# Optimization experiments

Hardware: AMD Instinct MI355X
Metric: run time of the kernel (lower is better)

## Reference

```python
import jax, jax.numpy as jnp
import numpy as np

FIR_KERNEL = (1, 3, 3, 1)
FACTOR = 2


def _setup_kernel(k):
    k = np.asarray(k, dtype=np.float32)
    if k.ndim == 1:
        k = np.outer(k, k)
    k /= np.sum(k)
    return k


def _fir_filter_2d(x, kf, pad0, pad1):
    # upfirdn2d with up=down=1: pad then depthwise-correlate with flipped FIR kernel.
    # x: [N, H, W, C], kf: [kh, kw]
    C = x.shape[3]
    x = jnp.pad(x, ((0, 0), (max(pad0, 0), max(pad1, 0)), (max(pad0, 0), max(pad1, 0)), (0, 0)))
    x = x[:, max(-pad0, 0): x.shape[1] - max(-pad1, 0), max(-pad0, 0): x.shape[2] - max(-pad1, 0), :]
    w = jnp.tile(jnp.asarray(kf[::-1, ::-1], x.dtype)[:, :, None, None], (1, 1, 1, C))
    return jax.lax.conv_general_dilated(
        x, w, window_strides=(1, 1), padding='VALID',
        dimension_numbers=('NHWC', 'HWIO', 'NHWC'), feature_group_count=C)


def _upsample_conv_2d(x, w, k, factor=2, gain=1.0):
    # StyleGAN2 fused upsample + conv: transposed 3x3 conv (stride=factor) then FIR filter.
    convH, convW, inC, outC = w.shape
    kf = _setup_kernel(k) * (gain * (factor ** 2))
    p = (kf.shape[0] - factor) - (convW - 1)
    num_groups = x.shape[3] // inC  # == 1 here
    # weight transform exactly as in up_or_down_sampling.upsample_conv_2d
    w = jnp.reshape(w, (convH, convW, inC, num_groups, -1))
    w = jnp.transpose(w[::-1, ::-1], (0, 1, 4, 3, 2))  # [cH, cW, outC, g, inC]
    w = jnp.reshape(w, (convH, convW, -1, num_groups * inC))
    x = jax.lax.conv_transpose(
        x, w, strides=(factor, factor), padding='VALID',
        transpose_kernel=True, dimension_numbers=('NHWC', 'HWIO', 'NHWC'))
    # [N, (H-1)*f+cH, (W-1)*f+cW, outC] -> FIR -> [N, 2H, 2W, outC]
    return _fir_filter_2d(x, kf, pad0=(p + 1) // 2 + factor - 1, pad1=p // 2 + 1)


def setup_inputs() -> dict:
    key = jax.random.key(0)
    k1, k2 = jax.random.split(key, 2)
    B, H, W, C = 4, 128, 128, 256
    out_ch = 256
    x = jax.random.normal(k1, (B, H, W, C), dtype=jnp.float32)
    # default_init(): variance_scaling(1., 'fan_avg', 'uniform')
    fan_avg = (3 * 3 * C + 3 * 3 * out_ch) / 2.0
    lim = float(np.sqrt(3.0 / fan_avg))
    w = jax.random.uniform(k2, (3, 3, C, out_ch), dtype=jnp.float32, minval=-lim, maxval=lim)
    b = jnp.zeros((out_ch,), dtype=jnp.float32)
    return {"x": x, "w": w, "b": b}


def reference(x, w, b):
    h = _upsample_conv_2d(x, w, FIR_KERNEL, factor=FACTOR)
    h = h + b.reshape(1, 1, 1, -1)
    return h
```

## Files before the change

### kernel.cpp

```cpp
#include <hip/hip_runtime.h>
#include <hip/hip_bf16.h>


typedef __attribute__((ext_vector_type(8))) __bf16 bf16x8;
typedef __attribute__((ext_vector_type(4))) float floatx4;

#define XP_ELEMS (4*130*130*256)
#define XP_BYTES (XP_ELEMS*2)
#define KT_ELEMS (1024*2304)

__device__ __forceinline__ void gl_lds16(const void* g, void* l) {
  __builtin_amdgcn_global_load_lds((const __attribute__((address_space(1))) void*)g,
                                   (__attribute__((address_space(3))) void*)l,
                                   16, 0, 0);
}

__global__ void pad_cast_kernel(const float* __restrict__ x,
                                __hip_bfloat16* __restrict__ xp) {
  int t = blockIdx.x * 256 + threadIdx.x;
  if (t >= 4*130*130*32) return;
  int c8  = (t & 31) << 3;
  int pix = t >> 5;
  int wc  = pix % 130;
  int tmp = pix / 130;
  int hr  = tmp % 130;
  int b   = tmp / 130;
  float vals[8] = {0.f,0.f,0.f,0.f,0.f,0.f,0.f,0.f};
  if (hr >= 1 && hr <= 128 && wc >= 1 && wc <= 128) {
    const float* s = x + (size_t)(((b*128 + (hr-1))*128 + (wc-1))*256 + c8);
    const float4 a = *(const float4*)s;
    const float4 c = *(const float4*)(s + 4);
    vals[0]=a.x; vals[1]=a.y; vals[2]=a.z; vals[3]=a.w;
    vals[4]=c.x; vals[5]=c.y; vals[6]=c.z; vals[7]=c.w;
  }
  __align__(16) __hip_bfloat16 o[8];
  #pragma unroll
  for (int i = 0; i < 8; ++i) o[i] = __float2bfloat16(vals[i]);
  *reinterpret_cast<uint4*>(xp + (size_t)t*8) = *reinterpret_cast<const uint4*>(o);
}

__global__ void make_kt_kernel(const float* __restrict__ w,
                               __hip_bfloat16* __restrict__ kt) {
  int t = blockIdx.x * 256 + threadIdx.x;
  if (t >= KT_ELEMS) return;
  int k = t % 2304;
  int n = t / 2304;
  int par = n >> 8, co = n & 255;
  int pr = par >> 1, ps = par & 1;
  int tap = k >> 8, ci = k & 255;
  int dy = tap / 3, dx = tap - dy*3;
  const float Atab[2][3][3] = {
    {{3.f,1.f,0.f},{1.f,3.f,3.f},{0.f,0.f,1.f}},
    {{1.f,0.f,0.f},{3.f,3.f,1.f},{0.f,1.f,3.f}}
  };
  float s = 0.f;
  #pragma unroll
  for (int i = 0; i < 3; ++i) {
    float ay = Atab[pr][dy][i];
    #pragma unroll
    for (int j = 0; j < 3; ++j) {
      float ax = Atab[ps][dx][j];
      float c = ay * ax;
      if (c != 0.f)
        s += c * w[(size_t)(((i*3 + j)*256 + ci))*256 + co];
    }
  }
  kt[t] = __float2bfloat16(s * 0.0625f);
}

__global__ __launch_bounds__(256) void gemm_kernel(
    const __hip_bfloat16* __restrict__ xp,
    const __hip_bfloat16* __restrict__ kt,
    const float* __restrict__ bias,
    float* __restrict__ out)
{
  __shared__ __align__(16) __hip_bfloat16 sA[128*32];
  __shared__ __align__(16) __hip_bfloat16 sB[128*32];

  const int tid = threadIdx.x;
  const int bid = blockIdx.x;
  const int mt  = bid >> 3;
  const int nt  = bid & 7;
  const int b   = mt >> 7;
  const int ro  = mt & 127;
  const int n0  = nt << 7;

  const int wv   = tid >> 6;
  const int ln   = tid & 63;
  const int lm   = ln & 15;
  const int quad = ln >> 4;
  const int wm   = wv >> 1;
  const int wn   = wv & 1;

  const int sr    = tid >> 2;
  const int inner = (tid & 3) << 3;

  __hip_bfloat16* lA0 = sA + (wv*64)*8;
  __hip_bfloat16* lA1 = sA + (wv*64 + 256)*8;
  __hip_bfloat16* lB0 = sB + (wv*64)*8;
  __hip_bfloat16* lB1 = sB + (wv*64 + 256)*8;

  floatx4 acc[4][4];
  #pragma unroll
  for (int i = 0; i < 4; ++i)
    #pragma unroll
    for (int j = 0; j < 4; ++j)
      acc[i][j] = (floatx4){0.f, 0.f, 0.f, 0.f};

  const __hip_bfloat16* xb = xp + (size_t)(b*130)*130*256;

  for (int ks = 0; ks < 72; ++ks) {
    const int tap = ks >> 3;
    const int ci0 = (ks & 7) << 5;
    const int dy  = tap / 3;
    const int dx  = tap - dy*3;
    const int k0  = ks << 5;

    const __hip_bfloat16* gA = xb + (size_t)((ro + dy)*130 + dx + sr)*256 + ci0 + inner;
    gl_lds16(gA,            lA0);
    gl_lds16(gA + 64*256,   lA1);
    const __hip_bfloat16* gB = kt + (size_t)(n0 + sr)*2304 + k0 + inner;
    gl_lds16(gB,            lB0);
    gl_lds16(gB + 64*2304,  lB1);

    __syncthreads();

    bf16x8 af[4], bfr[4];
    #pragma unroll
    for (int i = 0; i < 4; ++i)
      af[i]  = *reinterpret_cast<const bf16x8*>(sA + (wm*64 + i*16 + lm)*32 + quad*8);
    #pragma unroll
    for (int i = 0; i < 4; ++i)
      bfr[i] = *reinterpret_cast<const bf16x8*>(sB + (wn*64 + i*16 + lm)*32 + quad*8);

    #pragma unroll
    for (int mi = 0; mi < 4; ++mi)
      #pragma unroll
      for (int ni = 0; ni < 4; ++ni)
        acc[mi][ni] = __builtin_amdgcn_mfma_f32_16x16x32_bf16(af[mi], bfr[ni], acc[mi][ni], 0, 0, 0);

    __syncthreads();
  }

  #pragma unroll
  for (int ni = 0; ni < 4; ++ni) {
    const int n   = n0 + wn*64 + ni*16 + lm;
    const int par = n >> 8;
    const int co  = n & 255;
    const int pr  = par >> 1;
    const int ps  = par & 1;
    const float bv = bias[co];
    const int rowo = b*256 + 2*ro + pr;
    #pragma unroll
    for (int mi = 0; mi < 4; ++mi) {
      const int so_b = wm*64 + mi*16 + (quad << 2);
      #pragma unroll
      for (int r = 0; r < 4; ++r) {
        const int so = so_b + r;
        out[((size_t)rowo*256 + (2*so + ps))*256 + co] = acc[mi][ni][r] + bv;
      }
    }
  }
}

extern "C" void kernel_launch(void* const* d_in, const int* in_sizes, int n_in,
                              void* d_out, int out_size, void* d_ws, size_t ws_size,
                              hipStream_t stream) {
  const float* x    = (const float*)d_in[0];
  const float* w    = (const float*)d_in[1];
  const float* bias = (const float*)d_in[2];
  float* out = (float*)d_out;

  __hip_bfloat16* xp = (__hip_bfloat16*)d_ws;
  __hip_bfloat16* kt = (__hip_bfloat16*)((char*)d_ws + XP_BYTES);

  pad_cast_kernel<<<(4*130*130*32 + 255)/256, 256, 0, stream>>>(x, xp);
  make_kt_kernel<<<(KT_ELEMS + 255)/256, 256, 0, stream>>>(w, kt);
  gemm_kernel<<<4096, 256, 0, stream>>>(xp, kt, bias, out);
}
```

Measured before the change: 719.1 us.

## Swizzle LDS tiles, remap GEMM block order, and restructure weight-transform kernel

Applies an XOR swizzle to the LDS column offset for both the global-to-LDS writes and the fragment reads, to cut bank conflicts on the bf16x8 loads. Remaps block IDs so the eight N-tiles sharing a group of M-tiles run close together, improving L2 reuse of the activation rows. Rewrites the weight-transform kernel so each thread computes 32 contiguous input channels with coalesced weight reads and 16-byte stores, replacing the strided per-element scheme. The swizzle must stay consistent between the write and read paths.

```diff
diff --git a/kernel.cpp b/kernel.cpp
--- a/kernel.cpp
+++ b/kernel.cpp
@@ -41,31 +41,43 @@
 
 __global__ void make_kt_kernel(const float* __restrict__ w,
                                __hip_bfloat16* __restrict__ kt) {
-  int t = blockIdx.x * 256 + threadIdx.x;
-  if (t >= KT_ELEMS) return;
-  int k = t % 2304;
-  int n = t / 2304;
-  int par = n >> 8, co = n & 255;
-  int pr = par >> 1, ps = par & 1;
-  int tap = k >> 8, ci = k & 255;
-  int dy = tap / 3, dx = tap - dy*3;
+  const int b     = blockIdx.x;
+  const int ciblk = b & 7;
+  const int tap   = (b >> 3) % 9;
+  const int par   = b / 72;
+  const int co    = threadIdx.x;
+  const int pr = par >> 1, ps = par & 1;
+  const int dy = tap / 3, dx = tap - dy*3;
+
   const float Atab[2][3][3] = {
     {{3.f,1.f,0.f},{1.f,3.f,3.f},{0.f,0.f,1.f}},
     {{1.f,0.f,0.f},{3.f,3.f,1.f},{0.f,1.f,3.f}}
   };
-  float s = 0.f;
+
+  float s[32];
   #pragma unroll
+  for (int u = 0; u < 32; ++u) s[u] = 0.f;
+
   for (int i = 0; i < 3; ++i) {
-    float ay = Atab[pr][dy][i];
-    #pragma unroll
+    const float ay = Atab[pr][dy][i];
+    if (ay == 0.f) continue;
     for (int j = 0; j < 3; ++j) {
-      float ax = Atab[ps][dx][j];
-      float c = ay * ax;
-      if (c != 0.f)
-        s += c * w[(size_t)(((i*3 + j)*256 + ci))*256 + co];
+      const float c = ay * Atab[ps][dx][j];
+      if (c == 0.f) continue;
+      const float* wp = w + ((size_t)(i*3 + j)*256 + ciblk*32)*256 + co;
+      #pragma unroll
+      for (int u = 0; u < 32; ++u)
+        s[u] += c * wp[(size_t)u*256];
     }
   }
-  kt[t] = __float2bfloat16(s * 0.0625f);
+
+  __align__(16) __hip_bfloat16 o[32];
+  #pragma unroll
+  for (int u = 0; u < 32; ++u) o[u] = __float2bfloat16(s[u] * 0.0625f);
+  __hip_bfloat16* dst = kt + (size_t)(par*256 + co)*2304 + tap*256 + ciblk*32;
+  #pragma unroll
+  for (int v = 0; v < 4; ++v)
+    reinterpret_cast<uint4*>(dst)[v] = reinterpret_cast<const uint4*>(o)[v];
 }
 
 __global__ __launch_bounds__(256) void gemm_kernel(
@@ -79,8 +91,8 @@
 
   const int tid = threadIdx.x;
   const int bid = blockIdx.x;
-  const int mt  = bid >> 3;
-  const int nt  = bid & 7;
+  const int mt  = (bid & 7) + ((bid >> 6) << 3);
+  const int nt  = (bid >> 3) & 7;
   const int b   = mt >> 7;
   const int ro  = mt & 127;
   const int n0  = nt << 7;
@@ -93,7 +105,7 @@
   const int wn   = wv & 1;
 
   const int sr    = tid >> 2;
-  const int inner = (tid & 3) << 3;
+  const int inner = (((tid & 3) ^ ((sr >> 1) & 3)) << 3);
 
   __hip_bfloat16* lA0 = sA + (wv*64)*8;
   __hip_bfloat16* lA1 = sA + (wv*64 + 256)*8;
@@ -108,6 +120,7 @@
       acc[i][j] = (floatx4){0.f, 0.f, 0.f, 0.f};
 
   const __hip_bfloat16* xb = xp + (size_t)(b*130)*130*256;
+  const int cs = ((quad ^ ((lm >> 1) & 3)) << 3);
 
   for (int ks = 0; ks < 72; ++ks) {
     const int tap = ks >> 3;
@@ -128,10 +141,10 @@
     bf16x8 af[4], bfr[4];
     #pragma unroll
     for (int i = 0; i < 4; ++i)
-      af[i]  = *reinterpret_cast<const bf16x8*>(sA + (wm*64 + i*16 + lm)*32 + quad*8);
+      af[i]  = *reinterpret_cast<const bf16x8*>(sA + (wm*64 + i*16 + lm)*32 + cs);
     #pragma unroll
     for (int i = 0; i < 4; ++i)
-      bfr[i] = *reinterpret_cast<const bf16x8*>(sB + (wn*64 + i*16 + lm)*32 + quad*8);
+      bfr[i] = *reinterpret_cast<const bf16x8*>(sB + (wn*64 + i*16 + lm)*32 + cs);
 
     #pragma unroll
     for (int mi = 0; mi < 4; ++mi)
@@ -175,6 +188,6 @@
   __hip_bfloat16* kt = (__hip_bfloat16*)((char*)d_ws + XP_BYTES);
 
   pad_cast_kernel<<<(4*130*130*32 + 255)/256, 256, 0, stream>>>(x, xp);
-  make_kt_kernel<<<(KT_ELEMS + 255)/256, 256, 0, stream>>>(w, kt);
+  make_kt_kernel<<<288, 256, 0, stream>>>(w, kt);
   gemm_kernel<<<4096, 256, 0, stream>>>(xp, kt, bias, out);
 }
```

After: 638.5 us. 1.13x faster.
